# Performance work log

Hardware: AMD Instinct MI355X
Metric: run time of the kernel (lower is better)

The kernel has to match this reference:

```python
import jax, jax.numpy as jnp
import numpy as np

N = 131072      # octree nodes at this depth
C_IN = 256      # in_channels == out_channels
C_B = 64        # bottleneck channels = out_channels // 4
K = 27          # 3x3x3 octree kernel neighborhood
EPS = 1e-5


def _bn(x, g, b, m, v):
    # inference-style BatchNorm with given running stats
    return (x - m) * (g * jax.lax.rsqrt(v + EPS)) + b


def setup_inputs() -> dict:
    key = jax.random.key(0)
    ks = jax.random.split(key, 20)
    inp = {
        "data": jax.random.normal(ks[0], (N, C_IN), dtype=jnp.float32),
        "neigh": jax.random.randint(ks[1], (N, K), 0, N, dtype=jnp.int32),
        "depth": 6,
        # conv1x1a (Linear, no bias) + BN
        "w1": jax.random.normal(ks[2], (C_IN, C_B), dtype=jnp.float32) * 0.05,
        "bn1_g": jax.random.uniform(ks[3], (C_B,), dtype=jnp.float32) + 0.5,
        "bn1_b": jax.random.normal(ks[4], (C_B,), dtype=jnp.float32) * 0.1,
        "bn1_m": jax.random.normal(ks[5], (C_B,), dtype=jnp.float32) * 0.1,
        "bn1_v": jax.random.uniform(ks[6], (C_B,), dtype=jnp.float32) + 0.5,
        # octree conv3x3 (27-neighbor gather + GEMM, no bias) + BN
        "w3": jax.random.normal(ks[7], (K, C_B, C_B), dtype=jnp.float32) * 0.02,
        "bn2_g": jax.random.uniform(ks[8], (C_B,), dtype=jnp.float32) + 0.5,
        "bn2_b": jax.random.normal(ks[9], (C_B,), dtype=jnp.float32) * 0.1,
        "bn2_m": jax.random.normal(ks[10], (C_B,), dtype=jnp.float32) * 0.1,
        "bn2_v": jax.random.uniform(ks[11], (C_B,), dtype=jnp.float32) + 0.5,
        # conv1x1b + BN (no ReLU)
        "w2": jax.random.normal(ks[12], (C_B, C_IN), dtype=jnp.float32) * 0.05,
        "bn3_g": jax.random.uniform(ks[13], (C_IN,), dtype=jnp.float32) + 0.5,
        "bn3_b": jax.random.normal(ks[14], (C_IN,), dtype=jnp.float32) * 0.1,
        "bn3_m": jax.random.normal(ks[15], (C_IN,), dtype=jnp.float32) * 0.1,
        "bn3_v": jax.random.uniform(ks[16], (C_IN,), dtype=jnp.float32) + 0.5,
    }
    return inp


def reference(data, neigh, depth, w1, bn1_g, bn1_b, bn1_m, bn1_v,
              w3, bn2_g, bn2_b, bn2_m, bn2_v,
              w2, bn3_g, bn3_b, bn3_m, bn3_v):
    # conv1x1a + BN + ReLU
    c1 = jax.nn.relu(_bn(data @ w1, bn1_g, bn1_b, bn1_m, bn1_v))  # [N, C_B]
    # octree conv3x3: gather 27 neighbors then contract with [K, C_B, C_B]
    gathered = c1[neigh]                                          # [N, K, C_B]
    c2 = jnp.einsum('nkc,kcd->nd', gathered, w3)                  # [N, C_B]
    c2 = jax.nn.relu(_bn(c2, bn2_g, bn2_b, bn2_m, bn2_v))
    # conv1x1b + BN (no relu)
    c3 = _bn(c2 @ w2, bn3_g, bn3_b, bn3_m, bn3_v)                 # [N, C_IN]
    # residual (in_channels == out_channels -> identity shortcut) + ReLU
    return jax.nn.relu(c3 + data)
```

## Files before the change

### kernel.cpp

```cpp
#include <hip/hip_runtime.h>

#define NN 131072
#define CIN 256
#define CB 64
#define KNB 27

typedef __attribute__((ext_vector_type(8))) short short8_t;
typedef __attribute__((ext_vector_type(4))) float f32x4;

__device__ inline unsigned short f2bf(float f) {
    union { float f; unsigned u; } x; x.f = f;
    unsigned r = x.u + 0x7fffu + ((x.u >> 16) & 1u);
    return (unsigned short)(r >> 16);
}

__device__ inline f32x4 mfma16(short8_t a, short8_t b, f32x4 c) {
    return __builtin_amdgcn_mfma_f32_16x16x32_bf16(a, b, c, 0, 0, 0);
}

__global__ __launch_bounds__(256) void prep_kernel(
    const float* __restrict__ w1, const float* __restrict__ w3, const float* __restrict__ w2,
    const float* __restrict__ g1, const float* __restrict__ b1, const float* __restrict__ m1, const float* __restrict__ v1,
    const float* __restrict__ g2, const float* __restrict__ b2, const float* __restrict__ m2, const float* __restrict__ v2,
    const float* __restrict__ g3, const float* __restrict__ b3, const float* __restrict__ m3, const float* __restrict__ v3,
    unsigned short* __restrict__ w1p, unsigned short* __restrict__ w3p, unsigned short* __restrict__ w2p,
    float* __restrict__ bias1, float* __restrict__ bias2, float* __restrict__ bias3)
{
    int t = blockIdx.x * 256 + threadIdx.x;
    if (t < 16384) {
        int j = t & 7, lane = (t >> 3) & 63, tt = (t >> 9) & 3, s = t >> 11;
        int c = s * 32 + (lane >> 4) * 8 + j;
        int d = tt * 16 + (lane & 15);
        float sc = g1[d] * rsqrtf(v1[d] + 1e-5f);
        w1p[t] = f2bf(w1[c * CB + d] * sc);
    } else if (t < 16384 + 110592) {
        int u = t - 16384;
        int j = u & 7, lane = (u >> 3) & 63, tt = (u >> 9) & 3, s = (u >> 11) & 1, k = u >> 12;
        int c = s * 32 + (lane >> 4) * 8 + j;
        int d = tt * 16 + (lane & 15);
        float sc = g2[d] * rsqrtf(v2[d] + 1e-5f);
        w3p[u] = f2bf(w3[(k * CB + c) * CB + d] * sc);
    } else if (t < 143360) {
        int u = t - 126976;
        int j = u & 7, lane = (u >> 3) & 63, mt = (u >> 9) & 15, s = u >> 13;
        int c = s * 32 + (lane >> 4) * 8 + j;
        int d = mt * 16 + (lane & 15);
        float sc = g3[d] * rsqrtf(v3[d] + 1e-5f);
        w2p[u] = f2bf(w2[c * CIN + d] * sc);
    } else if (t < 143744) {
        int u = t - 143360;
        if (u < 64)       { float sc = g1[u] * rsqrtf(v1[u] + 1e-5f); bias1[u] = b1[u] - m1[u] * sc; }
        else if (u < 128) { int d = u - 64;  float sc = g2[d] * rsqrtf(v2[d] + 1e-5f); bias2[d] = b2[d] - m2[d] * sc; }
        else              { int d = u - 128; float sc = g3[d] * rsqrtf(v3[d] + 1e-5f); bias3[d] = b3[d] - m3[d] * sc; }
    }
}

__global__ __launch_bounds__(256) void k1_conv1x1a(
    const float* __restrict__ data, const unsigned short* __restrict__ w1p,
    const float* __restrict__ bias1, unsigned short* __restrict__ c1b)
{
    __shared__ short8_t w1s[2048];
    int tid = threadIdx.x;
    const short8_t* wsrc = (const short8_t*)w1p;
#pragma unroll
    for (int i = 0; i < 8; i++) w1s[tid + i * 256] = wsrc[tid + i * 256];

    int lane = tid & 63, wave = tid >> 6;
    int g = lane >> 4, r = lane & 15;
    int rowbase = blockIdx.x * 128 + wave * 32;
    f32x4 acc[2][4] = {};
    __syncthreads();

#pragma unroll
    for (int s = 0; s < 8; s++) {
        short8_t a[2];
#pragma unroll
        for (int sub = 0; sub < 2; sub++) {
            const float* ap = data + (size_t)(rowbase + sub * 16 + r) * CIN + s * 32 + g * 8;
            float4 f0 = *(const float4*)ap;
            float4 f1 = *(const float4*)(ap + 4);
            short8_t av;
            av[0] = (short)f2bf(f0.x); av[1] = (short)f2bf(f0.y);
            av[2] = (short)f2bf(f0.z); av[3] = (short)f2bf(f0.w);
            av[4] = (short)f2bf(f1.x); av[5] = (short)f2bf(f1.y);
            av[6] = (short)f2bf(f1.z); av[7] = (short)f2bf(f1.w);
            a[sub] = av;
        }
#pragma unroll
        for (int t = 0; t < 4; t++) {
            short8_t b = w1s[(s * 4 + t) * 64 + lane];
            acc[0][t] = mfma16(a[0], b, acc[0][t]);
            acc[1][t] = mfma16(a[1], b, acc[1][t]);
        }
    }

#pragma unroll
    for (int sub = 0; sub < 2; sub++)
#pragma unroll
        for (int t = 0; t < 4; t++) {
            int col = t * 16 + r;
            float bs = bias1[col];
#pragma unroll
            for (int i = 0; i < 4; i++) {
                int row = rowbase + sub * 16 + g * 4 + i;
                c1b[row * CB + col] = f2bf(fmaxf(acc[sub][t][i] + bs, 0.f));
            }
        }
}

#define KCLAMP(x) ((x) < 26 ? (x) : 26)

#define K2_LOADB(bN, kc) { \
    const short8_t* bp_ = bbase + (size_t)(kc) * 512; \
    bN[0] = bp_[lane];       bN[1] = bp_[64 + lane]; \
    bN[2] = bp_[128 + lane]; bN[3] = bp_[192 + lane]; \
    bN[4] = bp_[256 + lane]; bN[5] = bp_[320 + lane]; \
    bN[6] = bp_[384 + lane]; bN[7] = bp_[448 + lane]; }

#define K2_GATH(aN, kc) { \
    int i0_ = nidx[lr0 * KNB + (kc)]; \
    int i1_ = nidx[lr1 * KNB + (kc)]; \
    const short8_t* p0_ = (const short8_t*)(c1b + (size_t)i0_ * CB); \
    const short8_t* p1_ = (const short8_t*)(c1b + (size_t)i1_ * CB); \
    aN[0] = p0_[g]; aN[1] = p0_[4 + g]; aN[2] = p1_[g]; aN[3] = p1_[4 + g]; }

#define K2_MF(aC, bC) { \
    _Pragma("unroll") for (int t = 0; t < 4; t++) { \
        acc[0][t] = mfma16(aC[0], bC[t],     acc[0][t]); \
        acc[1][t] = mfma16(aC[2], bC[t],     acc[1][t]); \
        acc[0][t] = mfma16(aC[1], bC[4 + t], acc[0][t]); \
        acc[1][t] = mfma16(aC[3], bC[4 + t], acc[1][t]); } }

#define K2_STEP(aC, bC, aN, bN, k) \
    K2_LOADB(bN, KCLAMP((k) + 1)) \
    K2_GATH(aN, KCLAMP((k) + 2)) \
    K2_MF(aC, bC)

__global__ __launch_bounds__(64, 4) void k2_conv3x3(
    const unsigned short* __restrict__ c1b, const int* __restrict__ neigh,
    const unsigned short* __restrict__ w3p, const float* __restrict__ bias2,
    unsigned short* __restrict__ c2b)
{
    __shared__ int nidx[32 * KNB];
    int tid = threadIdx.x;
    int rowbase = blockIdx.x * 32;

    const int4* nsrc = (const int4*)(neigh + (size_t)rowbase * KNB);
#pragma unroll
    for (int i = 0; i < 4; i++) {
        int p = tid + i * 64;
        if (p < 216) ((int4*)nidx)[p] = nsrc[p];
    }

    int lane = tid & 63;
    int g = lane >> 4, r = lane & 15;
    int lr0 = r, lr1 = 16 + r;
    __syncthreads();

    const short8_t* bbase = (const short8_t*)w3p;
    f32x4 acc[2][4] = {};
    short8_t aA[4], aB[4], aC[4], bX[8], bY[8];

    K2_LOADB(bX, 0)
    K2_GATH(aA, 0)
    K2_GATH(aB, 1)

    for (int kb = 0; kb < 24; kb += 6) {
        K2_STEP(aA, bX, aC, bY, kb + 0)
        K2_STEP(aB, bY, aA, bX, kb + 1)
        K2_STEP(aC, bX, aB, bY, kb + 2)
        K2_STEP(aA, bY, aC, bX, kb + 3)
        K2_STEP(aB, bX, aA, bY, kb + 4)
        K2_STEP(aC, bY, aB, bX, kb + 5)
    }
    K2_STEP(aA, bX, aC, bY, 24)
    K2_STEP(aB, bY, aA, bX, 25)
    K2_STEP(aC, bX, aB, bY, 26)

#pragma unroll
    for (int sub = 0; sub < 2; sub++)
#pragma unroll
        for (int t = 0; t < 4; t++) {
            int col = t * 16 + r;
            float bs = bias2[col];
#pragma unroll
            for (int i = 0; i < 4; i++) {
                int row = rowbase + sub * 16 + g * 4 + i;
                c2b[row * CB + col] = f2bf(fmaxf(acc[sub][t][i] + bs, 0.f));
            }
        }
}

__global__ __launch_bounds__(256) void k3_conv1x1b(
    const unsigned short* __restrict__ c2b, const unsigned short* __restrict__ w2p,
    const float* __restrict__ bias3, const float* __restrict__ data,
    float* __restrict__ out)
{
    int tid = threadIdx.x;
    int lane = tid & 63, wave = tid >> 6;
    int g = lane >> 4, r = lane & 15;
    int rowbase = blockIdx.x * 32;

    const short8_t* abase = (const short8_t*)w2p;
    short8_t bfr[2][2];
#pragma unroll
    for (int sub = 0; sub < 2; sub++)
#pragma unroll
        for (int s = 0; s < 2; s++)
            bfr[sub][s] = *(const short8_t*)(c2b + (size_t)(rowbase + sub * 16 + r) * CB + s * 32 + g * 8);

    f32x4 acc2[2][4] = {};
#pragma unroll
    for (int mt = 0; mt < 4; mt++) {
        short8_t a0 = abase[(wave * 4 + mt) * 64 + lane];
        short8_t a1 = abase[(16 + wave * 4 + mt) * 64 + lane];
        acc2[0][mt] = mfma16(a0, bfr[0][0], acc2[0][mt]);
        acc2[0][mt] = mfma16(a1, bfr[0][1], acc2[0][mt]);
        acc2[1][mt] = mfma16(a0, bfr[1][0], acc2[1][mt]);
        acc2[1][mt] = mfma16(a1, bfr[1][1], acc2[1][mt]);
    }

#pragma unroll
    for (int sub = 0; sub < 2; sub++)
#pragma unroll
        for (int mt = 0; mt < 4; mt++) {
            int col0 = (wave * 4 + mt) * 16 + g * 4;
            int rowg = rowbase + sub * 16 + r;
            float4 bs = *(const float4*)(bias3 + col0);
            float4 dv = *(const float4*)(data + (size_t)rowg * CIN + col0);
            f32x4 v = acc2[sub][mt];
            float4 res;
            res.x = fmaxf(v[0] + bs.x + dv.x, 0.f);
            res.y = fmaxf(v[1] + bs.y + dv.y, 0.f);
            res.z = fmaxf(v[2] + bs.z + dv.z, 0.f);
            res.w = fmaxf(v[3] + bs.w + dv.w, 0.f);
            *(float4*)(out + (size_t)rowg * CIN + col0) = res;
        }
}

extern "C" void kernel_launch(void* const* d_in, const int* in_sizes, int n_in,
                              void* d_out, int out_size, void* d_ws, size_t ws_size,
                              hipStream_t stream)
{
    const float* data = (const float*)d_in[0];
    const int* neigh  = (const int*)d_in[1];
    const float* w1 = (const float*)d_in[3];
    const float* g1 = (const float*)d_in[4];
    const float* b1 = (const float*)d_in[5];
    const float* m1 = (const float*)d_in[6];
    const float* v1 = (const float*)d_in[7];
    const float* w3 = (const float*)d_in[8];
    const float* g2 = (const float*)d_in[9];
    const float* b2 = (const float*)d_in[10];
    const float* m2 = (const float*)d_in[11];
    const float* v2 = (const float*)d_in[12];
    const float* w2 = (const float*)d_in[13];
    const float* g3 = (const float*)d_in[14];
    const float* b3 = (const float*)d_in[15];
    const float* m3 = (const float*)d_in[16];
    const float* v3 = (const float*)d_in[17];
    float* out = (float*)d_out;

    char* ws = (char*)d_ws;
    unsigned short* c1b = (unsigned short*)ws;
    unsigned short* c2b = (unsigned short*)(ws + 16777216);
    unsigned short* w1p = (unsigned short*)(ws + 33554432);
    unsigned short* w3p = (unsigned short*)(ws + 33554432 + 32768);
    unsigned short* w2p = (unsigned short*)(ws + 33554432 + 32768 + 221184);
    float* bias1 = (float*)(ws + 33554432 + 32768 + 221184 + 32768);
    float* bias2 = bias1 + 64;
    float* bias3 = bias1 + 128;

    int n = in_sizes[0] / CIN;

    hipLaunchKernelGGL(prep_kernel, dim3(562), dim3(256), 0, stream,
                       w1, w3, w2, g1, b1, m1, v1, g2, b2, m2, v2, g3, b3, m3, v3,
                       w1p, w3p, w2p, bias1, bias2, bias3);
    hipLaunchKernelGGL(k1_conv1x1a, dim3(n / 128), dim3(256), 0, stream, data, w1p, bias1, c1b);
    hipLaunchKernelGGL(k2_conv3x3,  dim3(n / 32),  dim3(64),  0, stream, c1b, neigh, w3p, bias2, c2b);
    hipLaunchKernelGGL(k3_conv1x1b, dim3(n / 32),  dim3(256), 0, stream, c2b, w2p, bias3, data, out);
}
```

Before: 187.7 us.

## Quantize conv3x3 gather to int8 with dynamic per-tensor scales and int8 MFMA

Quantizes c1 activations and the BN-folded w3 weights to int8 using per-tensor absolute-max scales computed on device, then runs the 27-neighbor conv with i32 16x16x64 int8 MFMA. This halves the bytes per gathered neighbor row and uses the higher int8 MFMA rate. The cost is extra kernels (zero, an amax reduction with atomics, an activation quantization pass) and a loss of precision from per-tensor int8 on activations. The conv1x1b kernel also grows its tile to 64 rows per block, and the workspace is reorganized so c2b aliases c1b.

```diff
diff --git a/kernel.cpp b/kernel.cpp
--- a/kernel.cpp
+++ b/kernel.cpp
@@ -1,30 +1,40 @@
 #include <hip/hip_runtime.h>
 
-#define NN 131072
 #define CIN 256
 #define CB 64
 #define KNB 27
 
 typedef __attribute__((ext_vector_type(8))) short short8_t;
 typedef __attribute__((ext_vector_type(4))) float f32x4;
+typedef __attribute__((ext_vector_type(4))) int   i32x4;
 
 __device__ inline unsigned short f2bf(float f) {
     union { float f; unsigned u; } x; x.f = f;
     unsigned r = x.u + 0x7fffu + ((x.u >> 16) & 1u);
     return (unsigned short)(r >> 16);
 }
-
+__device__ inline float bf2f(unsigned short h) {
+    union { unsigned u; float f; } x; x.u = ((unsigned)h) << 16; return x.f;
+}
 __device__ inline f32x4 mfma16(short8_t a, short8_t b, f32x4 c) {
     return __builtin_amdgcn_mfma_f32_16x16x32_bf16(a, b, c, 0, 0, 0);
 }
-
-__global__ __launch_bounds__(256) void prep_kernel(
+__device__ inline i32x4 mfma_i8(i32x4 a, i32x4 b, i32x4 c) {
+    return __builtin_amdgcn_mfma_i32_16x16x64_i8(a, b, c, 0, 0, 0);
+}
+
+__global__ __launch_bounds__(64) void zero_kernel(unsigned* __restrict__ amax) {
+    if (threadIdx.x < 4) amax[threadIdx.x] = 0u;
+}
+
+__global__ __launch_bounds__(256) void prep_a_kernel(
     const float* __restrict__ w1, const float* __restrict__ w3, const float* __restrict__ w2,
     const float* __restrict__ g1, const float* __restrict__ b1, const float* __restrict__ m1, const float* __restrict__ v1,
     const float* __restrict__ g2, const float* __restrict__ b2, const float* __restrict__ m2, const float* __restrict__ v2,
     const float* __restrict__ g3, const float* __restrict__ b3, const float* __restrict__ m3, const float* __restrict__ v3,
-    unsigned short* __restrict__ w1p, unsigned short* __restrict__ w3p, unsigned short* __restrict__ w2p,
-    float* __restrict__ bias1, float* __restrict__ bias2, float* __restrict__ bias3)
+    unsigned short* __restrict__ w1p, unsigned short* __restrict__ w2p,
+    float* __restrict__ bias1, float* __restrict__ bias2, float* __restrict__ bias3,
+    unsigned* __restrict__ amax)
 {
     int t = blockIdx.x * 256 + threadIdx.x;
     if (t < 16384) {
@@ -33,13 +43,14 @@
         int d = tt * 16 + (lane & 15);
         float sc = g1[d] * rsqrtf(v1[d] + 1e-5f);
         w1p[t] = f2bf(w1[c * CB + d] * sc);
-    } else if (t < 16384 + 110592) {
-        int u = t - 16384;
-        int j = u & 7, lane = (u >> 3) & 63, tt = (u >> 9) & 3, s = (u >> 11) & 1, k = u >> 12;
-        int c = s * 32 + (lane >> 4) * 8 + j;
-        int d = tt * 16 + (lane & 15);
+    } else if (t < 126976) {
+        int e = t - 16384;
+        int d = e & 63;
         float sc = g2[d] * rsqrtf(v2[d] + 1e-5f);
-        w3p[u] = f2bf(w3[(k * CB + c) * CB + d] * sc);
+        float m = fabsf(w3[e] * sc);
+#pragma unroll
+        for (int off = 32; off; off >>= 1) m = fmaxf(m, __shfl_xor(m, off));
+        if ((threadIdx.x & 63) == 0) atomicMax(&amax[1], __float_as_uint(m));
     } else if (t < 143360) {
         int u = t - 126976;
         int j = u & 7, lane = (u >> 3) & 63, mt = (u >> 9) & 15, s = u >> 13;
@@ -55,9 +66,26 @@
     }
 }
 
+__global__ __launch_bounds__(256) void prep_b_kernel(
+    const float* __restrict__ w3, const float* __restrict__ g2, const float* __restrict__ v2,
+    const unsigned* __restrict__ amax, signed char* __restrict__ w3q)
+{
+    int u = blockIdx.x * 256 + threadIdx.x;
+    int j = u & 15, lane = (u >> 4) & 63, tile = (u >> 10) & 3, k = u >> 12;
+    int c = (lane >> 4) * 16 + j;
+    int d = tile * 16 + (lane & 15);
+    float sw = __uint_as_float(amax[1]);
+    float inv = sw > 0.f ? 127.f / sw : 0.f;
+    float sc = g2[d] * rsqrtf(v2[d] + 1e-5f);
+    int q = __float2int_rn(w3[(k * CB + c) * CB + d] * sc * inv);
+    q = q > 127 ? 127 : (q < -127 ? -127 : q);
+    w3q[u] = (signed char)q;
+}
+
 __global__ __launch_bounds__(256) void k1_conv1x1a(
     const float* __restrict__ data, const unsigned short* __restrict__ w1p,
-    const float* __restrict__ bias1, unsigned short* __restrict__ c1b)
+    const float* __restrict__ bias1, unsigned short* __restrict__ c1b,
+    unsigned* __restrict__ amax)
 {
     __shared__ short8_t w1s[2048];
     int tid = threadIdx.x;
@@ -94,6 +122,7 @@
         }
     }
 
+    float mloc = 0.f;
 #pragma unroll
     for (int sub = 0; sub < 2; sub++)
 #pragma unroll
@@ -103,43 +132,45 @@
 #pragma unroll
             for (int i = 0; i < 4; i++) {
                 int row = rowbase + sub * 16 + g * 4 + i;
-                c1b[row * CB + col] = f2bf(fmaxf(acc[sub][t][i] + bs, 0.f));
+                float v = fmaxf(acc[sub][t][i] + bs, 0.f);
+                mloc = fmaxf(mloc, v);
+                c1b[row * CB + col] = f2bf(v);
             }
         }
-}
-
-#define KCLAMP(x) ((x) < 26 ? (x) : 26)
-
-#define K2_LOADB(bN, kc) { \
-    const short8_t* bp_ = bbase + (size_t)(kc) * 512; \
-    bN[0] = bp_[lane];       bN[1] = bp_[64 + lane]; \
-    bN[2] = bp_[128 + lane]; bN[3] = bp_[192 + lane]; \
-    bN[4] = bp_[256 + lane]; bN[5] = bp_[320 + lane]; \
-    bN[6] = bp_[384 + lane]; bN[7] = bp_[448 + lane]; }
-
-#define K2_GATH(aN, kc) { \
-    int i0_ = nidx[lr0 * KNB + (kc)]; \
-    int i1_ = nidx[lr1 * KNB + (kc)]; \
-    const short8_t* p0_ = (const short8_t*)(c1b + (size_t)i0_ * CB); \
-    const short8_t* p1_ = (const short8_t*)(c1b + (size_t)i1_ * CB); \
-    aN[0] = p0_[g]; aN[1] = p0_[4 + g]; aN[2] = p1_[g]; aN[3] = p1_[4 + g]; }
-
-#define K2_MF(aC, bC) { \
-    _Pragma("unroll") for (int t = 0; t < 4; t++) { \
-        acc[0][t] = mfma16(aC[0], bC[t],     acc[0][t]); \
-        acc[1][t] = mfma16(aC[2], bC[t],     acc[1][t]); \
-        acc[0][t] = mfma16(aC[1], bC[4 + t], acc[0][t]); \
-        acc[1][t] = mfma16(aC[3], bC[4 + t], acc[1][t]); } }
-
-#define K2_STEP(aC, bC, aN, bN, k) \
-    K2_LOADB(bN, KCLAMP((k) + 1)) \
-    K2_GATH(aN, KCLAMP((k) + 2)) \
-    K2_MF(aC, bC)
+#pragma unroll
+    for (int off = 32; off; off >>= 1) mloc = fmaxf(mloc, __shfl_xor(mloc, off));
+    if (lane == 0) atomicMax(&amax[0], __float_as_uint(mloc));
+}
+
+__global__ __launch_bounds__(256) void quant_c1_kernel(
+    const unsigned short* __restrict__ c1b, const unsigned* __restrict__ amax,
+    signed char* __restrict__ c1q)
+{
+    int t = blockIdx.x * 256 + threadIdx.x;
+    float s1 = __uint_as_float(amax[0]);
+    float inv = s1 > 0.f ? 127.f / s1 : 0.f;
+    const short8_t* src = (const short8_t*)c1b;
+    short8_t v0 = src[t * 2], v1 = src[t * 2 + 1];
+    int ow[4];
+#pragma unroll
+    for (int h = 0; h < 4; h++) {
+        int w = 0;
+#pragma unroll
+        for (int e = 0; e < 4; e++) {
+            unsigned short hv = (unsigned short)((h < 2 ? v0 : v1)[(h & 1) * 4 + e]);
+            int q = __float2int_rn(bf2f(hv) * inv);
+            q = q > 127 ? 127 : q;
+            w |= (q & 0xff) << (e * 8);
+        }
+        ow[h] = w;
+    }
+    ((int4*)c1q)[t] = make_int4(ow[0], ow[1], ow[2], ow[3]);
+}
 
 __global__ __launch_bounds__(64, 4) void k2_conv3x3(
-    const unsigned short* __restrict__ c1b, const int* __restrict__ neigh,
-    const unsigned short* __restrict__ w3p, const float* __restrict__ bias2,
-    unsigned short* __restrict__ c2b)
+    const signed char* __restrict__ c1q, const int* __restrict__ neigh,
+    const signed char* __restrict__ w3q, const float* __restrict__ bias2,
+    const unsigned* __restrict__ amax, unsigned short* __restrict__ c2b)
 {
     __shared__ int nidx[32 * KNB];
     int tid = threadIdx.x;
@@ -152,30 +183,33 @@
         if (p < 216) ((int4*)nidx)[p] = nsrc[p];
     }
 
-    int lane = tid & 63;
+    int lane = tid;
     int g = lane >> 4, r = lane & 15;
-    int lr0 = r, lr1 = 16 + r;
+    float sf = __uint_as_float(amax[0]) * __uint_as_float(amax[1]) * (1.f / (127.f * 127.f));
     __syncthreads();
 
-    const short8_t* bbase = (const short8_t*)w3p;
-    f32x4 acc[2][4] = {};
-    short8_t aA[4], aB[4], aC[4], bX[8], bY[8];
-
-    K2_LOADB(bX, 0)
-    K2_GATH(aA, 0)
-    K2_GATH(aB, 1)
-
-    for (int kb = 0; kb < 24; kb += 6) {
-        K2_STEP(aA, bX, aC, bY, kb + 0)
-        K2_STEP(aB, bY, aA, bX, kb + 1)
-        K2_STEP(aC, bX, aB, bY, kb + 2)
-        K2_STEP(aA, bY, aC, bX, kb + 3)
-        K2_STEP(aB, bX, aA, bY, kb + 4)
-        K2_STEP(aC, bY, aB, bX, kb + 5)
-    }
-    K2_STEP(aA, bX, aC, bY, 24)
-    K2_STEP(aB, bY, aA, bX, 25)
-    K2_STEP(aC, bX, aB, bY, 26)
+    const i32x4* bq = (const i32x4*)w3q;
+    i32x4 iacc[2][4] = {};
+
+#pragma unroll
+    for (int k = 0; k < KNB; k++) {
+        i32x4 b0 = bq[k * 256 + lane];
+        i32x4 b1 = bq[k * 256 + 64 + lane];
+        i32x4 b2 = bq[k * 256 + 128 + lane];
+        i32x4 b3 = bq[k * 256 + 192 + lane];
+        int i0 = nidx[r * KNB + k];
+        int i1 = nidx[(16 + r) * KNB + k];
+        i32x4 a0 = *(const i32x4*)(c1q + (size_t)i0 * CB + g * 16);
+        i32x4 a1 = *(const i32x4*)(c1q + (size_t)i1 * CB + g * 16);
+        iacc[0][0] = mfma_i8(a0, b0, iacc[0][0]);
+        iacc[1][0] = mfma_i8(a1, b0, iacc[1][0]);
+        iacc[0][1] = mfma_i8(a0, b1, iacc[0][1]);
+        iacc[1][1] = mfma_i8(a1, b1, iacc[1][1]);
+        iacc[0][2] = mfma_i8(a0, b2, iacc[0][2]);
+        iacc[1][2] = mfma_i8(a1, b2, iacc[1][2]);
+        iacc[0][3] = mfma_i8(a0, b3, iacc[0][3]);
+        iacc[1][3] = mfma_i8(a1, b3, iacc[1][3]);
+    }
 
 #pragma unroll
     for (int sub = 0; sub < 2; sub++)
@@ -186,7 +220,8 @@
 #pragma unroll
             for (int i = 0; i < 4; i++) {
                 int row = rowbase + sub * 16 + g * 4 + i;
-                c2b[row * CB + col] = f2bf(fmaxf(acc[sub][t][i] + bs, 0.f));
+                float v = fmaxf((float)iacc[sub][t][i] * sf + bs, 0.f);
+                c2b[row * CB + col] = f2bf(v);
             }
         }
 }
@@ -199,29 +234,29 @@
     int tid = threadIdx.x;
     int lane = tid & 63, wave = tid >> 6;
     int g = lane >> 4, r = lane & 15;
-    int rowbase = blockIdx.x * 32;
+    int rowbase = blockIdx.x * 64;
 
     const short8_t* abase = (const short8_t*)w2p;
-    short8_t bfr[2][2];
-#pragma unroll
-    for (int sub = 0; sub < 2; sub++)
+    short8_t bfr[4][2];
+#pragma unroll
+    for (int sub = 0; sub < 4; sub++)
 #pragma unroll
         for (int s = 0; s < 2; s++)
             bfr[sub][s] = *(const short8_t*)(c2b + (size_t)(rowbase + sub * 16 + r) * CB + s * 32 + g * 8);
 
-    f32x4 acc2[2][4] = {};
-#pragma unroll
-    for (int mt = 0; mt < 4; mt++) {
-        short8_t a0 = abase[(wave * 4 + mt) * 64 + lane];
-        short8_t a1 = abase[(16 + wave * 4 + mt) * 64 + lane];
-        acc2[0][mt] = mfma16(a0, bfr[0][0], acc2[0][mt]);
-        acc2[0][mt] = mfma16(a1, bfr[0][1], acc2[0][mt]);
-        acc2[1][mt] = mfma16(a0, bfr[1][0], acc2[1][mt]);
-        acc2[1][mt] = mfma16(a1, bfr[1][1], acc2[1][mt]);
-    }
-
-#pragma unroll
-    for (int sub = 0; sub < 2; sub++)
+    f32x4 acc2[4][4] = {};
+#pragma unroll
+    for (int s = 0; s < 2; s++)
+#pragma unroll
+        for (int mt = 0; mt < 4; mt++) {
+            short8_t a = abase[(s * 16 + wave * 4 + mt) * 64 + lane];
+#pragma unroll
+            for (int sub = 0; sub < 4; sub++)
+                acc2[sub][mt] = mfma16(a, bfr[sub][s], acc2[sub][mt]);
+        }
+
+#pragma unroll
+    for (int sub = 0; sub < 4; sub++)
 #pragma unroll
         for (int mt = 0; mt < 4; mt++) {
             int col0 = (wave * 4 + mt) * 16 + g * 4;
@@ -263,20 +298,30 @@
 
     char* ws = (char*)d_ws;
     unsigned short* c1b = (unsigned short*)ws;
-    unsigned short* c2b = (unsigned short*)(ws + 16777216);
-    unsigned short* w1p = (unsigned short*)(ws + 33554432);
-    unsigned short* w3p = (unsigned short*)(ws + 33554432 + 32768);
-    unsigned short* w2p = (unsigned short*)(ws + 33554432 + 32768 + 221184);
-    float* bias1 = (float*)(ws + 33554432 + 32768 + 221184 + 32768);
+    unsigned short* c2b = (unsigned short*)ws;
+    signed char*    c1q = (signed char*)(ws + 16777216);
+    unsigned short* w1p = (unsigned short*)(ws + 25165824);
+    signed char*    w3q = (signed char*)(ws + 25198592);
+    unsigned short* w2p = (unsigned short*)(ws + 25309184);
+    float* bias1 = (float*)(ws + 25341952);
     float* bias2 = bias1 + 64;
     float* bias3 = bias1 + 128;
+    unsigned* amax = (unsigned*)(ws + 25343488);
 
     int n = in_sizes[0] / CIN;
 
-    hipLaunchKernelGGL(prep_kernel, dim3(562), dim3(256), 0, stream,
+    hipLaunchKernelGGL(zero_kernel, dim3(1), dim3(64), 0, stream, amax);
+    hipLaunchKernelGGL(prep_a_kernel, dim3(562), dim3(256), 0, stream,
                        w1, w3, w2, g1, b1, m1, v1, g2, b2, m2, v2, g3, b3, m3, v3,
-                       w1p, w3p, w2p, bias1, bias2, bias3);
-    hipLaunchKernelGGL(k1_conv1x1a, dim3(n / 128), dim3(256), 0, stream, data, w1p, bias1, c1b);
-    hipLaunchKernelGGL(k2_conv3x3,  dim3(n / 32),  dim3(64),  0, stream, c1b, neigh, w3p, bias2, c2b);
-    hipLaunchKernelGGL(k3_conv1x1b, dim3(n / 32),  dim3(256), 0, stream, c2b, w2p, bias3, data, out);
-}
+                       w1p, w2p, bias1, bias2, bias3, amax);
+    hipLaunchKernelGGL(prep_b_kernel, dim3(432), dim3(256), 0, stream,
+                       w3, g2, v2, amax, w3q);
+    hipLaunchKernelGGL(k1_conv1x1a, dim3(n / 128), dim3(256), 0, stream,
+                       data, w1p, bias1, c1b, amax);
+    hipLaunchKernelGGL(quant_c1_kernel, dim3(2048), dim3(256), 0, stream,
+                       c1b, amax, c1q);
+    hipLaunchKernelGGL(k2_conv3x3, dim3(n / 32), dim3(64), 0, stream,
+                       c1q, neigh, w3q, bias2, amax, c2b);
+    hipLaunchKernelGGL(k3_conv1x1b, dim3(n / 64), dim3(256), 0, stream,
+                       c2b, w2p, bias3, data, out);
+}
```

New measurement: 219.6 us. 17.0% more time.
